# Kernel optimization log

Hardware: AMD Instinct MI355X
Metric: run time of the kernel (lower is better)

## Reference

```python
import jax, jax.numpy as jnp
import numpy as np

B = 2            # batch
T = 1_000_000    # texels per texture
C = 16           # channels
G = 500_000      # flattened groups
K = 9            # texels per group (mesh-neighborhood stencil)


def setup_inputs() -> dict:
    key = jax.random.key(0)
    k1, k2, k3 = jax.random.split(key, 3)
    mesh_ids = jax.random.randint(k1, (B,), 0, 4, dtype=jnp.int32)
    textures = jax.random.normal(k2, (B, T, C), dtype=jnp.float32)
    group_idx = jax.random.randint(k3, (G, K), 0, T, dtype=jnp.int32)
    return {"mesh_ids": mesh_ids, "textures": textures, "group_idx": group_idx}


def reference(mesh_ids, textures, group_idx):
    # Forward pass of textures_to_flattened_groups: gather per-texel features
    # into flattened mesh-connectivity groups.
    # textures: [B, T, C]; group_idx: [G, K] -> out: [B, G, K, C]
    out = jnp.take(textures, group_idx.reshape(-1), axis=1)  # [B, G*K, C]
    return out.reshape(textures.shape[0], G, K, textures.shape[-1])
```

## Files before the change

### kernel.cpp

```cpp
#include <hip/hip_runtime.h>


typedef float f4 __attribute__((ext_vector_type(4)));

constexpr long long T_ = 1000000;
constexpr int       C4 = 4;
constexpr long long GK = 500000LL * 9;

__global__ __launch_bounds__(256) void
TMSCNNTexturesToFlattenedGroups_74294344286542_kernel(
    const f4* __restrict__ textures,
    const int* __restrict__ group_idx,
    f4*       __restrict__ out)
{
    unsigned int tid = blockIdx.x * blockDim.x + threadIdx.x;
    const unsigned long long total = (unsigned long long)GK * C4;
    if (tid >= total) return;

    const int          c4 = tid & 3;
    const unsigned int gk = tid >> 2;

    const int idx = group_idx[gk];

    const long long src0 = (long long)idx * C4 + c4;
    const long long src1 = (T_ + (long long)idx) * C4 + c4;

    const f4 v0 = textures[src0];
    const f4 v1 = textures[src1];

    const long long dst0 = (long long)gk * C4 + c4;
    const long long dst1 = (GK + (long long)gk) * C4 + c4;

    __builtin_nontemporal_store(v0, &out[dst0]);
    __builtin_nontemporal_store(v1, &out[dst1]);
}

extern "C" void kernel_launch(void* const* d_in, const int* in_sizes, int n_in,
                              void* d_out, int out_size, void* d_ws, size_t ws_size,
                              hipStream_t stream) {
    const f4*  textures  = (const f4*)d_in[1];
    const int* group_idx = (const int*)d_in[2];
    f4*        out       = (f4*)d_out;

    const unsigned long long total = (unsigned long long)GK * C4;
    const int threads = 256;
    const int blocks  = (int)((total + threads - 1) / threads);

    TMSCNNTexturesToFlattenedGroups_74294344286542_kernel<<<blocks, threads, 0, stream>>>(
        textures, group_idx, out);
}
```

Measured before the change: 762.7 us.

## Repack textures to interleave batches per texel before gathering

Adds a repack pass into the workspace that stores both batch rows of each texel contiguously (128 bytes), so the gather reads one contiguous cache-line-sized chunk per index instead of two scattered 64-byte chunks. The gather then uses 8 threads per group element and writes to both batch halves of the output. The cost is an extra full pass over the 128 MB texture array on every call, plus a workspace requirement. It falls back to the direct kernel if the workspace is too small.

Measured after the change: 758.4 us. About the same (-0.6%).

```diff
diff --git a/kernel.cpp b/kernel.cpp
--- a/kernel.cpp
+++ b/kernel.cpp
@@ -6,31 +6,58 @@
 constexpr long long T_ = 1000000;
 constexpr int       C4 = 4;
 constexpr long long GK = 500000LL * 9;
+constexpr long long PACKED_F4 = T_ * 2 * C4;
 
 __global__ __launch_bounds__(256) void
-TMSCNNTexturesToFlattenedGroups_74294344286542_kernel(
-    const f4* __restrict__ textures,
-    const int* __restrict__ group_idx,
-    f4*       __restrict__ out)
+TMSCNN_repack_kernel(const f4* __restrict__ textures, f4* __restrict__ packed)
 {
-    unsigned int tid = blockIdx.x * blockDim.x + threadIdx.x;
-    const unsigned long long total = (unsigned long long)GK * C4;
-    if (tid >= total) return;
+    const unsigned tid = blockIdx.x * blockDim.x + threadIdx.x;
+    if (tid >= (unsigned)PACKED_F4) return;
+    const unsigned j   = tid & 7;
+    const unsigned t   = tid >> 3;
+    const unsigned b   = j >> 2;
+    const unsigned c4  = j & 3;
+    const long long src = ((long long)b * T_ + (long long)t) * C4 + c4;
+    packed[tid] = textures[src];
+}
 
+__global__ __launch_bounds__(256) void
+TMSCNN_gather_kernel(const f4* __restrict__ packed,
+                     const int* __restrict__ group_idx,
+                     f4*       __restrict__ out)
+{
+    const unsigned tid = blockIdx.x * blockDim.x + threadIdx.x;
+    if (tid >= (unsigned)(GK * 8)) return;
+    const unsigned j   = tid & 7;
+    const unsigned gk  = tid >> 3;
+    const unsigned b   = j >> 2;
+    const unsigned c4  = j & 3;
+
+    const int idx = __builtin_nontemporal_load(&group_idx[gk]);
+
+    const f4 v = packed[(long long)idx * 8 + j];
+
+    const long long dst = (long long)b * (GK * C4) + (long long)gk * C4 + c4;
+    __builtin_nontemporal_store(v, &out[dst]);
+}
+
+__global__ __launch_bounds__(256) void
+TMSCNN_direct_kernel(const f4* __restrict__ textures,
+                     const int* __restrict__ group_idx,
+                     f4*       __restrict__ out)
+{
+    const unsigned tid = blockIdx.x * blockDim.x + threadIdx.x;
+    if (tid >= (unsigned)(GK * C4)) return;
     const int          c4 = tid & 3;
     const unsigned int gk = tid >> 2;
 
     const int idx = group_idx[gk];
-
     const long long src0 = (long long)idx * C4 + c4;
     const long long src1 = (T_ + (long long)idx) * C4 + c4;
-
     const f4 v0 = textures[src0];
     const f4 v1 = textures[src1];
-
     const long long dst0 = (long long)gk * C4 + c4;
     const long long dst1 = (GK + (long long)gk) * C4 + c4;
-
     __builtin_nontemporal_store(v0, &out[dst0]);
     __builtin_nontemporal_store(v1, &out[dst1]);
 }
@@ -42,10 +69,22 @@
     const int* group_idx = (const int*)d_in[2];
     f4*        out       = (f4*)d_out;
 
-    const unsigned long long total = (unsigned long long)GK * C4;
     const int threads = 256;
-    const int blocks  = (int)((total + threads - 1) / threads);
+    const size_t packed_bytes = (size_t)PACKED_F4 * sizeof(f4);
 
-    TMSCNNTexturesToFlattenedGroups_74294344286542_kernel<<<blocks, threads, 0, stream>>>(
-        textures, group_idx, out);
+    if (d_ws != nullptr && ws_size >= packed_bytes) {
+        f4* packed = (f4*)d_ws;
+
+        const long long nA = PACKED_F4;
+        const long long nB = GK * 8;
+
+        TMSCNN_repack_kernel<<<(int)((nA + threads - 1) / threads), threads, 0, stream>>>(
+            textures, packed);
+        TMSCNN_gather_kernel<<<(int)((nB + threads - 1) / threads), threads, 0, stream>>>(
+            packed, group_idx, out);
+    } else {
+        const unsigned long long total = (unsigned long long)GK * C4;
+        TMSCNN_direct_kernel<<<(int)((total + threads - 1) / threads), threads, 0, stream>>>(
+            textures, group_idx, out);
+    }
 }
```
